# Kernel tuning notes

Measured on AMD Instinct MI355X. Metric: run time of the kernel, lower is better.

The kernel has to match this reference:

```python
import jax, jax.numpy as jnp
import numpy as np


def setup_inputs() -> dict:
    key = jax.random.key(0)
    ks = jax.random.split(key, 9)
    N, C, SY, SX = 256, 128, 11, 25
    DM, DC, D = 64, 64, 128
    return {
        "f_t_global": jax.random.normal(ks[0], (N, D), dtype=jnp.float32),
        "x_t_local": jax.random.normal(ks[1], (N, C, SY, SX), dtype=jnp.float32),
        "x_t_prev_local": jax.random.normal(ks[2], (N, C, SY, SX), dtype=jnp.float32),
        "m_t": jax.random.normal(ks[3], (N, DM), dtype=jnp.float32),
        "m_t_prev": jax.random.normal(ks[4], (N, DM), dtype=jnp.float32),
        "c_t": jax.random.normal(ks[5], (N, DC), dtype=jnp.float32),
        "c_t_prev": jax.random.normal(ks[6], (N, DC), dtype=jnp.float32),
        "W_join": jax.random.normal(ks[7], (C + DM + DC, D), dtype=jnp.float32) * 0.05,
        "b_join": jax.random.normal(ks[8], (D,), dtype=jnp.float32) * 0.05,
    }


def reference(f_t_global, x_t_local, x_t_prev_local, m_t, m_t_prev, c_t, c_t_prev, W_join, b_join):
    N, C, SY, SX = x_t_local.shape
    P = SY * SX
    DM = m_t.shape[1]
    # join_obs(local, m, c) = concat([local, m, c]) @ W_join + b_join, split for efficiency
    Wl = W_join[:C]                 # [C, D]
    Wm = W_join[C:C + DM]           # [DM, D]
    Wc = W_join[C + DM:]            # [DC, D]
    # [N, C, SY, SX] -> [P, N, C]: all spatial positions batched at once
    loc_t = x_t_local.reshape(N, C, P).transpose(2, 0, 1)
    loc_p = x_t_prev_local.reshape(N, C, P).transpose(2, 0, 1)
    bias_t = m_t @ Wm + c_t @ Wc + b_join             # [N, D], shared across positions
    bias_p = m_t_prev @ Wm + c_t_prev @ Wc + b_join   # [N, D]
    positive = jnp.einsum('pnc,cd->pnd', loc_p, Wl) + bias_p[None]  # [P, N, D]
    pred_loc = jnp.einsum('pnc,cd->pnd', loc_t, Wl) + bias_t[None]  # [P, N, D]

    # loss1: global prediction vs per-position prev-local positives
    logits1 = jnp.einsum('nd,pmd->pnm', f_t_global, positive)   # [P, N, N]
    # loss2: per-position current-local vs per-position prev-local
    logits2 = jnp.einsum('pnd,pmd->pnm', pred_loc, positive)    # [P, N, N]

    def mean_infonce(logits):
        # cross_entropy(logits, arange(N)) averaged over batch, then over positions
        lse = jax.nn.logsumexp(logits, axis=-1)            # [P, N]
        diag = jnp.diagonal(logits, axis1=1, axis2=2)      # [P, N]
        return jnp.mean(lse - diag)

    loss1 = mean_infonce(logits1)
    loss2 = mean_infonce(logits2)
    return loss1 + loss2
```

## Files before the change

kernel.cpp:

```cpp
#include <hip/hip_runtime.h>

#define Nn 256
#define Cc 128
#define Pp 275
#define Dd 128

typedef unsigned int u32;
typedef unsigned short u16;
typedef float f32x4 __attribute__((ext_vector_type(4)));
typedef short bf16x8 __attribute__((ext_vector_type(8)));

__device__ __forceinline__ float bf2f(u16 h) {
    return __uint_as_float(((u32)h) << 16);
}
__device__ __forceinline__ u16 f2bf(float f) {
    u32 u = __float_as_uint(f);
    return (u16)((u + 0x7fffu + ((u >> 16) & 1u)) >> 16);
}

__global__ __launch_bounds__(256) void bias_kernel(
    const float* __restrict__ m_t, const float* __restrict__ m_p,
    const float* __restrict__ c_t, const float* __restrict__ c_p,
    const float* __restrict__ W, const float* __restrict__ b,
    const float* __restrict__ f,
    float* __restrict__ bias_t, float* __restrict__ bias_p,
    u16* __restrict__ f_bf, u16* __restrict__ WlT)
{
    int idx = blockIdx.x * 256 + threadIdx.x;
    int n = idx >> 7, d = idx & 127;
    float at = 0.f, ap = 0.f;
#pragma unroll 8
    for (int k = 0; k < 64; ++k) {
        float wm = W[(128 + k) * 128 + d];
        float wc = W[(192 + k) * 128 + d];
        at = fmaf(m_t[n * 64 + k], wm, at);
        at = fmaf(c_t[n * 64 + k], wc, at);
        ap = fmaf(m_p[n * 64 + k], wm, ap);
        ap = fmaf(c_p[n * 64 + k], wc, ap);
    }
    float bb = b[d];
    bias_t[idx] = at + bb;
    bias_p[idx] = ap + bb;
    f_bf[idx] = f2bf(f[idx]);
    if (idx < 16384) {
        int dd = idx >> 7, cc = idx & 127;
        WlT[idx] = f2bf(W[cc * 128 + dd]);
    }
}

__global__ __launch_bounds__(512) void join_dbuf_kernel(
    const float* __restrict__ x_t, const float* __restrict__ x_p,
    const u16* __restrict__ WlT,
    const float* __restrict__ bias_t, const float* __restrict__ bias_p,
    u16* __restrict__ pred, u16* __restrict__ pos)
{
    __shared__ u16 wlds[128 * 128];
    __shared__ u16 xlds[2][2][16 * 128];
    const int tid = threadIdx.x;
    const int half = blockIdx.x;
    const int n = blockIdx.y;
    const int w = tid >> 6;
    const int l = tid & 63;
    const int g = l >> 4;

    {
        const uint4* src = reinterpret_cast<const uint4*>(WlT);
#pragma unroll
        for (int it = 0; it < 4; ++it) {
            int j = tid + 512 * it;
            int row = j >> 4;
            int colb = (j & 15) << 4;
            uint4 v = src[j];
            *reinterpret_cast<uint4*>((char*)wlds + row * 256 + (colb ^ ((row & 7) << 4))) = v;
        }
    }

    const int sq = tid & 255;
    const int spass = tid >> 8;
    const int sc0 = (sq >> 2) * 2;
    const int sp4 = (sq & 3) << 2;
    const float* sx = (spass ? x_p : x_t) + (size_t)n * (Cc * Pp);

    const int cpass = w & 1;
    const int dt0 = w >> 1;
    const float* bias = cpass ? bias_p : bias_t;
    u16* outp = cpass ? pos : pred;
    const float bv0 = bias[n * 128 + dt0 * 16 + (l & 15)];
    const float bv1 = bias[n * 128 + (dt0 + 4) * 16 + (l & 15)];

    {
        const int ch = half * 9;
        const int p0 = (ch < 17) ? ch * 16 : 259;
        const float* a = sx + (size_t)sc0 * Pp + p0 + sp4;
        f32x4 t0 = *reinterpret_cast<const f32x4*>(a);
        f32x4 t1 = *reinterpret_cast<const f32x4*>(a + Pp);
#pragma unroll
        for (int e = 0; e < 4; ++e) {
            const int row = sp4 + e;
            u32 pk = (u32)f2bf(t0[e]) | ((u32)f2bf(t1[e]) << 16);
            *reinterpret_cast<u32*>((char*)&xlds[0][spass][0]
                + row * 256 + ((sc0 * 2) ^ ((row & 7) << 4))) = pk;
        }
    }
    __syncthreads();

    int ib = 0;
    for (int tt = 0; tt < 9; ++tt) {
        const int ch = half * 9 + tt;
        const int p0 = (ch < 17) ? ch * 16 : 259;

        f32x4 t0, t1;
        const bool have = (tt < 8);
        if (have) {
            const int chn = ch + 1;
            const int pn0 = (chn < 17) ? chn * 16 : 259;
            const float* a = sx + (size_t)sc0 * Pp + pn0 + sp4;
            t0 = *reinterpret_cast<const f32x4*>(a);
            t1 = *reinterpret_cast<const f32x4*>(a + Pp);
        }

        const char* ab = (const char*)&xlds[ib][cpass][0];
        const int arow = l & 15;
        bf16x8 A[4];
#pragma unroll
        for (int kk = 0; kk < 4; ++kk)
            A[kk] = *reinterpret_cast<const bf16x8*>(
                ab + arow * 256 + ((kk * 64 + g * 16) ^ ((arow & 7) << 4)));

#pragma unroll
        for (int i = 0; i < 2; ++i) {
            const int dt = dt0 + i * 4;
            bf16x8 B[4];
            const int row = dt * 16 + (l & 15);
#pragma unroll
            for (int kk = 0; kk < 4; ++kk) {
                int cbyte = kk * 64 + (g << 4);
                B[kk] = *reinterpret_cast<const bf16x8*>(
                    (const char*)wlds + row * 256 + (cbyte ^ ((row & 7) << 4)));
            }
            f32x4 acc = {0.f, 0.f, 0.f, 0.f};
#pragma unroll
            for (int kk = 0; kk < 4; ++kk)
                acc = __builtin_amdgcn_mfma_f32_16x16x32_bf16(A[kk], B[kk], acc, 0, 0, 0);
            const int d = dt * 16 + (l & 15);
            const float bv = i ? bv1 : bv0;
#pragma unroll
            for (int r = 0; r < 4; ++r) {
                const int p = p0 + g * 4 + r;
                outp[((size_t)p * Nn + n) * Dd + d] = f2bf(acc[r] + bv);
            }
        }

        if (have) {
#pragma unroll
            for (int e = 0; e < 4; ++e) {
                const int row = sp4 + e;
                u32 pk = (u32)f2bf(t0[e]) | ((u32)f2bf(t1[e]) << 16);
                *reinterpret_cast<u32*>((char*)&xlds[ib ^ 1][spass][0]
                    + row * 256 + ((sc0 * 2) ^ ((row & 7) << 4))) = pk;
            }
        }
        __syncthreads();
        ib ^= 1;
    }
}

__global__ __launch_bounds__(512) void logits_part_kernel(
    const u16* __restrict__ f_bf,
    const u16* __restrict__ pred, const u16* __restrict__ pos,
    float* __restrict__ spart, float* __restrict__ dgarr)
{
    __shared__ u16 lds[128 * Dd];
    const int tid = threadIdx.x;
    const int sel = blockIdx.x >> 1;
    const int mhalf = blockIdx.x & 1;
    const int p = blockIdx.y;
    const int w = tid >> 6;
    const int l = tid & 63;
    const int r0 = w * 32;

    {
        const uint4* src = reinterpret_cast<const uint4*>(
            pos + (size_t)p * (Nn * Dd) + (size_t)mhalf * 128 * Dd);
#pragma unroll
        for (int it = 0; it < 4; ++it) {
            int j = tid + 512 * it;
            int row = j >> 4;
            int colb = (j & 15) << 4;
            uint4 v = src[j];
            *reinterpret_cast<uint4*>((char*)lds + row * 256 + (colb ^ ((row & 7) << 4))) = v;
        }
    }

    const u16* Abase = sel ? (pred + (size_t)p * (Nn * Dd)) : f_bf;
    bf16x8 A[2][4];
    {
        const int arow = l & 15;
        const int acol = (l >> 4) << 4;
#pragma unroll
        for (int rt = 0; rt < 2; ++rt)
#pragma unroll
            for (int kk = 0; kk < 4; ++kk) {
                const char* ap = (const char*)Abase
                               + (size_t)(r0 + rt * 16 + arow) * 256 + kk * 64 + acol;
                A[rt][kk] = *reinterpret_cast<const bf16x8*>(ap);
            }
    }

    __syncthreads();

    const float L2E = 1.4426950408889634f;
    float s_[2][4];
    float dg[2][4];
#pragma unroll
    for (int rt = 0; rt < 2; ++rt)
#pragma unroll
        for (int r = 0; r < 4; ++r) { s_[rt][r] = 0.f; dg[rt][r] = 0.f; }

    const int mcol = l & 15;
    const int bcol = (l >> 4) << 4;

    for (int ctl = 0; ctl < 8; ++ctl) {
        bf16x8 B[4];
        const int mrow = ctl * 16 + mcol;
#pragma unroll
        for (int kk = 0; kk < 4; ++kk) {
            int cb = kk * 64 + bcol;
            B[kk] = *reinterpret_cast<const bf16x8*>(
                (const char*)lds + mrow * 256 + (cb ^ ((mrow & 7) << 4)));
        }
#pragma unroll
        for (int rt = 0; rt < 2; ++rt) {
            f32x4 acc = {0.f, 0.f, 0.f, 0.f};
#pragma unroll
            for (int kk = 0; kk < 4; ++kk)
                acc = __builtin_amdgcn_mfma_f32_16x16x32_bf16(A[rt][kk], B[kk], acc, 0, 0, 0);
            const bool isdg_ct = ((mhalf * 8 + ctl) == ((r0 >> 4) + rt));
#pragma unroll
            for (int r = 0; r < 4; ++r) {
                float v = acc[r];
                s_[rt][r] += __builtin_amdgcn_exp2f(fmaf(v, L2E, -64.f));
                if (isdg_ct && ((l & 15) == (((l >> 4) << 2) + r))) dg[rt][r] = v;
            }
        }
    }

    float* sp = spart + (((size_t)(sel * Pp + p) * 2 + mhalf) << 8);
    float* dp = dgarr + (((size_t)(sel * Pp + p)) << 8);
    const bool owns_dg = ((w >> 2) == mhalf);
#pragma unroll
    for (int rt = 0; rt < 2; ++rt)
#pragma unroll
        for (int r = 0; r < 4; ++r) {
            float s = s_[rt][r];
            s += __shfl_xor(s, 1);
            s += __shfl_xor(s, 2);
            s += __shfl_xor(s, 4);
            s += __shfl_xor(s, 8);
            if ((l & 15) == (((l >> 4) << 2) + r)) {
                const int n = r0 + rt * 16 + ((l >> 4) << 2) + r;
                sp[n] = s;
                if (owns_dg) dp[n] = dg[rt][r];
            }
        }
}

__global__ __launch_bounds__(256) void merge_kernel(
    const float* __restrict__ spart, const float* __restrict__ dgarr,
    float* __restrict__ partial)
{
    __shared__ float red[256];
    const int sel = blockIdx.x;
    const int p = blockIdx.y;
    const int n = threadIdx.x;
    const size_t base = ((size_t)(sel * Pp + p) * 2) << 8;
    float s = spart[base + n] + spart[base + 256 + n];
    float dgv = dgarr[(((size_t)(sel * Pp + p)) << 8) + n];
    float val = 0.6931471805599453f * (64.f + __log2f(s)) - dgv;
    red[n] = val;
    __syncthreads();
    for (int k = 128; k > 0; k >>= 1) {
        if (n < k) red[n] += red[n + k];
        __syncthreads();
    }
    if (n == 0) partial[sel * Pp + p] = red[0];
}

__global__ __launch_bounds__(256) void reduce_kernel(
    const float* __restrict__ partial, float* __restrict__ out)
{
    __shared__ float red[256];
    float s = 0.f;
    for (int i = threadIdx.x; i < 2 * Pp; i += 256) s += partial[i];
    red[threadIdx.x] = s;
    __syncthreads();
    for (int k = 128; k > 0; k >>= 1) {
        if (threadIdx.x < k) red[threadIdx.x] += red[threadIdx.x + k];
        __syncthreads();
    }
    if (threadIdx.x == 0) out[0] = red[0] * (1.0f / (Pp * (float)Nn));
}

extern "C" void kernel_launch(void* const* d_in, const int* in_sizes, int n_in,
                              void* d_out, int out_size, void* d_ws, size_t ws_size,
                              hipStream_t stream)
{
    const float* f   = (const float*)d_in[0];
    const float* x_t = (const float*)d_in[1];
    const float* x_p = (const float*)d_in[2];
    const float* m_t = (const float*)d_in[3];
    const float* m_p = (const float*)d_in[4];
    const float* c_t = (const float*)d_in[5];
    const float* c_p = (const float*)d_in[6];
    const float* W   = (const float*)d_in[7];
    const float* b   = (const float*)d_in[8];

    char* ws = (char*)d_ws;
    const size_t SLAB = (size_t)Pp * Nn * Dd;

    float* bias_t = (float*)ws;
    float* bias_p = bias_t + Nn * Dd;
    u16* f_bf = (u16*)(ws + 262144);
    u16* WlT  = f_bf + Nn * Dd;
    u16* pred = (u16*)(ws + 360448);
    u16* pos  = pred + SLAB;
    float* partial = (float*)(pos + SLAB);
    float* spart   = partial + 2 * Pp;
    float* dgarr   = spart + (size_t)2 * Pp * 2 * 256;

    bias_kernel<<<dim3(Nn * Dd / 256), 256, 0, stream>>>(m_t, m_p, c_t, c_p, W, b, f,
                                                         bias_t, bias_p, f_bf, WlT);
    join_dbuf_kernel<<<dim3(2, Nn), 512, 0, stream>>>(x_t, x_p, WlT, bias_t, bias_p,
                                                      pred, pos);
    logits_part_kernel<<<dim3(4, Pp), 512, 0, stream>>>(f_bf, pred, pos, spart, dgarr);
    merge_kernel<<<dim3(2, Pp), 256, 0, stream>>>(spart, dgarr, partial);
    reduce_kernel<<<1, 256, 0, stream>>>(partial, (float*)d_out);
}
```

Before: 67.47 us.

## Stage full per-sample slab in LDS and keep weights in registers for join

The join kernel now assigns one block per (input tensor, sample) instead of splitting positions into halves. Each block loads all 275 positions for its sample into LDS in one pass using a new XOR swizzle. Each wave keeps its 16 weight columns in registers, read directly from global memory instead of staging the whole weight matrix in LDS. This removes the double-buffered chunk loop and its per-chunk barriers, at the cost of a ~70KB LDS footprint that limits occupancy and no overlap between loading and compute.

```diff
diff --git a/kernel.cpp b/kernel.cpp
--- a/kernel.cpp
+++ b/kernel.cpp
@@ -48,120 +48,84 @@
     }
 }
 
-__global__ __launch_bounds__(512) void join_dbuf_kernel(
+__global__ __launch_bounds__(512) void join_full_kernel(
     const float* __restrict__ x_t, const float* __restrict__ x_p,
     const u16* __restrict__ WlT,
     const float* __restrict__ bias_t, const float* __restrict__ bias_p,
     u16* __restrict__ pred, u16* __restrict__ pos)
 {
-    __shared__ u16 wlds[128 * 128];
-    __shared__ u16 xlds[2][2][16 * 128];
+    __shared__ u16 xlds[275 * 128];
     const int tid = threadIdx.x;
-    const int half = blockIdx.x;
+    const int pass = blockIdx.x;
     const int n = blockIdx.y;
     const int w = tid >> 6;
     const int l = tid & 63;
     const int g = l >> 4;
 
+    const float* sx = (pass ? x_p : x_t) + (size_t)n * (Cc * Pp);
+    u16* outp = pass ? pos : pred;
+
+    bf16x8 B[4];
     {
-        const uint4* src = reinterpret_cast<const uint4*>(WlT);
-#pragma unroll
-        for (int it = 0; it < 4; ++it) {
-            int j = tid + 512 * it;
-            int row = j >> 4;
-            int colb = (j & 15) << 4;
-            uint4 v = src[j];
-            *reinterpret_cast<uint4*>((char*)wlds + row * 256 + (colb ^ ((row & 7) << 4))) = v;
-        }
-    }
-
-    const int sq = tid & 255;
-    const int spass = tid >> 8;
-    const int sc0 = (sq >> 2) * 2;
-    const int sp4 = (sq & 3) << 2;
-    const float* sx = (spass ? x_p : x_t) + (size_t)n * (Cc * Pp);
-
-    const int cpass = w & 1;
-    const int dt0 = w >> 1;
-    const float* bias = cpass ? bias_p : bias_t;
-    u16* outp = cpass ? pos : pred;
-    const float bv0 = bias[n * 128 + dt0 * 16 + (l & 15)];
-    const float bv1 = bias[n * 128 + (dt0 + 4) * 16 + (l & 15)];
+        const int row = w * 16 + (l & 15);
+#pragma unroll
+        for (int kk = 0; kk < 4; ++kk)
+            B[kk] = *reinterpret_cast<const bf16x8*>(
+                (const char*)WlT + row * 256 + kk * 64 + g * 16);
+    }
+    const float bv = (pass ? bias_p : bias_t)[n * 128 + w * 16 + (l & 15)];
 
     {
-        const int ch = half * 9;
-        const int p0 = (ch < 17) ? ch * 16 : 259;
-        const float* a = sx + (size_t)sc0 * Pp + p0 + sp4;
-        f32x4 t0 = *reinterpret_cast<const f32x4*>(a);
-        f32x4 t1 = *reinterpret_cast<const f32x4*>(a + Pp);
-#pragma unroll
-        for (int e = 0; e < 4; ++e) {
-            const int row = sp4 + e;
-            u32 pk = (u32)f2bf(t0[e]) | ((u32)f2bf(t1[e]) << 16);
-            *reinterpret_cast<u32*>((char*)&xlds[0][spass][0]
-                + row * 256 + ((sc0 * 2) ^ ((row & 7) << 4))) = pk;
+        const int c0 = (tid >> 3) * 2;
+        const int j = tid & 7;
+        const float* r0p = sx + (size_t)c0 * Pp;
+        const float* r1p = r0p + Pp;
+        for (int q = j; q < 69; q += 8) {
+            const int pbase = 4 * q;
+            float v0[4], v1[4];
+            if (q < 68) {
+                f32x4 t0 = *reinterpret_cast<const f32x4*>(r0p + pbase);
+                f32x4 t1 = *reinterpret_cast<const f32x4*>(r1p + pbase);
+#pragma unroll
+                for (int e = 0; e < 4; ++e) { v0[e] = t0[e]; v1[e] = t1[e]; }
+            } else {
+#pragma unroll
+                for (int e = 0; e < 4; ++e) {
+                    int pe = pbase + e; if (pe > Pp - 1) pe = Pp - 1;
+                    v0[e] = r0p[pe]; v1[e] = r1p[pe];
+                }
+            }
+#pragma unroll
+            for (int e = 0; e < 4; ++e) {
+                int p = pbase + e; if (p > Pp - 1) p = Pp - 1;
+                const int col = (c0 * 2) ^ ((p & 7) << 4) ^ (((p >> 3) & 1) << 5);
+                *reinterpret_cast<u32*>((char*)xlds + p * 256 + col) =
+                    (u32)f2bf(v0[e]) | ((u32)f2bf(v1[e]) << 16);
+            }
         }
     }
     __syncthreads();
 
-    int ib = 0;
-    for (int tt = 0; tt < 9; ++tt) {
-        const int ch = half * 9 + tt;
-        const int p0 = (ch < 17) ? ch * 16 : 259;
-
-        f32x4 t0, t1;
-        const bool have = (tt < 8);
-        if (have) {
-            const int chn = ch + 1;
-            const int pn0 = (chn < 17) ? chn * 16 : 259;
-            const float* a = sx + (size_t)sc0 * Pp + pn0 + sp4;
-            t0 = *reinterpret_cast<const f32x4*>(a);
-            t1 = *reinterpret_cast<const f32x4*>(a + Pp);
-        }
-
-        const char* ab = (const char*)&xlds[ib][cpass][0];
-        const int arow = l & 15;
+    const int d = w * 16 + (l & 15);
+#pragma unroll
+    for (int t = 0; t < 18; ++t) {
+        const int p0 = (t < 17) ? t * 16 : 259;
+        const int arow = p0 + (l & 15);
         bf16x8 A[4];
 #pragma unroll
+        for (int kk = 0; kk < 4; ++kk) {
+            const int col = (kk * 64 + g * 16) ^ ((arow & 7) << 4) ^ (((arow >> 3) & 1) << 5);
+            A[kk] = *reinterpret_cast<const bf16x8*>((const char*)xlds + arow * 256 + col);
+        }
+        f32x4 acc = {0.f, 0.f, 0.f, 0.f};
+#pragma unroll
         for (int kk = 0; kk < 4; ++kk)
-            A[kk] = *reinterpret_cast<const bf16x8*>(
-                ab + arow * 256 + ((kk * 64 + g * 16) ^ ((arow & 7) << 4)));
-
-#pragma unroll
-        for (int i = 0; i < 2; ++i) {
-            const int dt = dt0 + i * 4;
-            bf16x8 B[4];
-            const int row = dt * 16 + (l & 15);
-#pragma unroll
-            for (int kk = 0; kk < 4; ++kk) {
-                int cbyte = kk * 64 + (g << 4);
-                B[kk] = *reinterpret_cast<const bf16x8*>(
-                    (const char*)wlds + row * 256 + (cbyte ^ ((row & 7) << 4)));
-            }
-            f32x4 acc = {0.f, 0.f, 0.f, 0.f};
-#pragma unroll
-            for (int kk = 0; kk < 4; ++kk)
-                acc = __builtin_amdgcn_mfma_f32_16x16x32_bf16(A[kk], B[kk], acc, 0, 0, 0);
-            const int d = dt * 16 + (l & 15);
-            const float bv = i ? bv1 : bv0;
-#pragma unroll
-            for (int r = 0; r < 4; ++r) {
-                const int p = p0 + g * 4 + r;
-                outp[((size_t)p * Nn + n) * Dd + d] = f2bf(acc[r] + bv);
-            }
-        }
-
-        if (have) {
-#pragma unroll
-            for (int e = 0; e < 4; ++e) {
-                const int row = sp4 + e;
-                u32 pk = (u32)f2bf(t0[e]) | ((u32)f2bf(t1[e]) << 16);
-                *reinterpret_cast<u32*>((char*)&xlds[ib ^ 1][spass][0]
-                    + row * 256 + ((sc0 * 2) ^ ((row & 7) << 4))) = pk;
-            }
-        }
-        __syncthreads();
-        ib ^= 1;
+            acc = __builtin_amdgcn_mfma_f32_16x16x32_bf16(A[kk], B[kk], acc, 0, 0, 0);
+#pragma unroll
+        for (int r = 0; r < 4; ++r) {
+            const int p = p0 + g * 4 + r;
+            outp[((size_t)p * Nn + n) * Dd + d] = f2bf(acc[r] + bv);
+        }
     }
 }
 
@@ -258,9 +222,9 @@
             s += __shfl_xor(s, 4);
             s += __shfl_xor(s, 8);
             if ((l & 15) == (((l >> 4) << 2) + r)) {
-                const int n = r0 + rt * 16 + ((l >> 4) << 2) + r;
-                sp[n] = s;
-                if (owns_dg) dp[n] = dg[rt][r];
+                const int nn = r0 + rt * 16 + ((l >> 4) << 2) + r;
+                sp[nn] = s;
+                if (owns_dg) dp[nn] = dg[rt][r];
             }
         }
 }
@@ -330,7 +294,7 @@
 
     bias_kernel<<<dim3(Nn * Dd / 256), 256, 0, stream>>>(m_t, m_p, c_t, c_p, W, b, f,
                                                          bias_t, bias_p, f_bf, WlT);
-    join_dbuf_kernel<<<dim3(2, Nn), 512, 0, stream>>>(x_t, x_p, WlT, bias_t, bias_p,
+    join_full_kernel<<<dim3(2, Nn), 512, 0, stream>>>(x_t, x_p, WlT, bias_t, bias_p,
                                                       pred, pos);
     logits_part_kernel<<<dim3(4, Pp), 512, 0, stream>>>(f_bf, pred, pos, spart, dgarr);
     merge_kernel<<<dim3(2, Pp), 256, 0, stream>>>(spart, dgarr, partial);
```

After: 62.74 us. 1.08x faster.
